# Optimization experiments

Measured on AMD Instinct MI355X. Metric: run time of the kernel, lower is better.

Reference implementation:

```python
import jax, jax.numpy as jnp
import numpy as np

N_UNITS = 512
N_HEADS = 8
CHUNK = N_UNITS // N_HEADS
SCALE = 1.0 / (CHUNK ** 0.5)


def setup_inputs() -> dict:
    key = jax.random.key(0)
    k1, k2, k3, k4, k5, k6 = jax.random.split(key, 6)
    B, Nx, Ny = 8, 1024, 1024
    x = jax.random.normal(k1, (B, N_UNITS, Nx), dtype=jnp.float32)
    y = jax.random.normal(k2, (B, N_UNITS, Ny), dtype=jnp.float32)
    xy_mask = jax.random.randint(k3, (B, Nx, Ny), 0, 2) > 0
    # conv1x1 weight [out, in] (ConvolutionSentence, bias=False)
    W = jax.random.normal(k4, (N_UNITS, N_UNITS), dtype=jnp.float32) * (1.0 / np.sqrt(N_UNITS))
    fc_w = jax.random.normal(k5, (1, N_HEADS), dtype=jnp.float32) * (1.0 / np.sqrt(N_HEADS))
    fc_b = jax.random.normal(k6, (1,), dtype=jnp.float32) * 0.01
    return {"x": x, "y": y, "xy_mask": xy_mask, "W": W, "fc_w": fc_w, "fc_b": fc_b}


def reference(x, y, xy_mask, W, fc_w, fc_b):
    B, U, Nx = x.shape
    Ny = y.shape[2]
    H, C = N_HEADS, CHUNK
    # 1x1 conv over channel dim == linear on channels
    _x = jnp.einsum('oi,bin->bon', W, x)  # [B, U, Nx]
    _y = jnp.einsum('oi,bim->bom', W, y)  # [B, U, Ny]
    # split channels into heads (contiguous chunks, matching torch.split)
    xh = _x.reshape(B, H, C, Nx)
    yh = _y.reshape(B, H, C, Ny)
    # per-head scores: relu, then scale, then mask (order matches torch code)
    s = jnp.einsum('bhcn,bhcm->bhnm', xh, yh)  # [B, H, Nx, Ny]
    s = jnp.maximum(s, 0.0) * SCALE
    s = jnp.where(xy_mask[:, None, :, :], s, 0.0)
    similarity = s.sum(axis=(2, 3))  # [B, H]
    n_el = xy_mask.sum(axis=(1, 2))
    n_el = jnp.where(n_el == 0, 1, n_el).astype(similarity.dtype)
    expectation = similarity / n_el[:, None]
    return expectation @ fc_w.T + fc_b  # [B, 1]
```

## Files before the change

kernel.cpp:

```cpp
#include <hip/hip_runtime.h>
#include <stdint.h>

#define UU 512
#define NHEAD 8
#define NB 8
#define NXX 1024
#define NYY 1024
#define SCALE_F 0.125f

typedef __bf16 bf16x8 __attribute__((ext_vector_type(8)));
typedef float f32x4 __attribute__((ext_vector_type(4)));
typedef unsigned short us4 __attribute__((ext_vector_type(4)));

__device__ __forceinline__ unsigned short f2bf(float f) {
  union { float f; uint32_t u; } v; v.f = f;
  return (unsigned short)((v.u + 0x7FFFu + ((v.u >> 16) & 1u)) >> 16);
}

__global__ void prep_kernel(const float* __restrict__ W, unsigned short* __restrict__ Wp,
                            const unsigned char* __restrict__ m, int* __restrict__ det) {
  int blk = blockIdx.x, t = threadIdx.x;
  if (blk < 128) {
    int s = blk * 256 + t;
    int ub = s >> 10, kb = (s >> 6) & 15, l = s & 63;
    int u = ub * 16 + (l & 15), k = kb * 32 + (l >> 4) * 8;
    const float* src = W + (size_t)u * UU + k;
    float4 a = *(const float4*)src;
    float4 bq = *(const float4*)(src + 4);
    uint4 o;
    o.x = (unsigned)f2bf(a.x) | ((unsigned)f2bf(a.y) << 16);
    o.y = (unsigned)f2bf(a.z) | ((unsigned)f2bf(a.w) << 16);
    o.z = (unsigned)f2bf(bq.x) | ((unsigned)f2bf(bq.y) << 16);
    o.w = (unsigned)f2bf(bq.z) | ((unsigned)f2bf(bq.w) << 16);
    *(uint4*)(Wp + (size_t)s * 8) = o;
  } else {
    int idx = ((blk - 128) * 256 + t) * 16;
    uint4 v = *(const uint4*)(m + idx);
    unsigned int c1 = (v.x & 0xff00u) | (v.y & 0xff00u) | (v.z & 0xff00u) | (v.w & 0xff00u);
    if (c1) atomicOr(&det[0], 1);
  }
}

__global__ __launch_bounds__(256, 2) void conv_fused(
    const float* __restrict__ x, const float* __restrict__ y,
    const unsigned short* __restrict__ Wp, unsigned short* __restrict__ pc) {
  __shared__ unsigned short xs[64 * 512];
  int fl = blockIdx.x;
  int bz = fl & 15, nt = (fl >> 4) & 15, ut = fl >> 8;
  int b = bz & 7;
  const float* src = (bz >> 3) ? y : x;
  int n0 = nt * 64;
  int t = threadIdx.x, w = t >> 6, l = t & 63;
  int lane_m = l & 15, lane_g = l >> 4;

  {
    int cq = (t & 15) * 4;
    int i2b = (t >> 4) * 2;
    const float* gb = src + (size_t)b * UU * NXX + n0 + cq;
#pragma unroll
    for (int it = 0; it < 16; it++) {
      int i2 = i2b + it * 32;
      float4 va = *(const float4*)(gb + (size_t)i2 * NXX);
      float4 vb = *(const float4*)(gb + (size_t)(i2 + 1) * NXX);
      float fa[4] = {va.x, va.y, va.z, va.w};
      float fb[4] = {vb.x, vb.y, vb.z, vb.w};
#pragma unroll
      for (int j = 0; j < 4; j++) {
        int n = cq + j;
        unsigned int pk = (unsigned)f2bf(fa[j]) | ((unsigned)f2bf(fb[j]) << 16);
        int e = n * 512 + (i2 ^ ((n & 7) << 3));
        *(unsigned int*)&xs[e] = pk;
      }
    }
  }
  __syncthreads();

  int u0 = ut * 256 + w * 64;
  int ub0 = u0 >> 4;
  const unsigned short* wb0 = Wp + (size_t)l * 8;
  f32x4 acc[4][4] = {};
  bf16x8 aA[4], aB[4], bA[4], bB[4];

#define LOADW(Adst, Bdst, KB) do {                                            \
    _Pragma("unroll") for (int tu = 0; tu < 4; tu++)                          \
      Adst[tu] = *(const bf16x8*)(wb0 + ((size_t)(ub0 + tu) * 16 + (KB)) * 512); \
    _Pragma("unroll") for (int tn = 0; tn < 4; tn++) {                        \
      int nl_ = tn * 16 + lane_m;                                             \
      int ka_ = (KB) * 32 + lane_g * 8;                                       \
      Bdst[tn] = *(const bf16x8*)&xs[nl_ * 512 + (ka_ ^ ((nl_ & 7) << 3))];   \
    }                                                                         \
  } while (0)
#define DOMFMA(Ab, Bb) do {                                                   \
    _Pragma("unroll") for (int tn = 0; tn < 4; tn++)                          \
    _Pragma("unroll") for (int tu = 0; tu < 4; tu++)                          \
      acc[tn][tu] = __builtin_amdgcn_mfma_f32_16x16x32_bf16(Ab[tu], Bb[tn], acc[tn][tu], 0, 0, 0); \
  } while (0)

  LOADW(aA, bA, 0);
#pragma unroll
  for (int kp = 0; kp < 8; kp++) {
    LOADW(aB, bB, 2 * kp + 1);
    DOMFMA(aA, bA);
    if (kp < 7) LOADW(aA, bA, 2 * kp + 2);
    DOMFMA(aB, bB);
  }
#undef LOADW
#undef DOMFMA

  unsigned short* ob = pc + (size_t)bz * 64 * 8 * 2 * 512;
  int h = u0 >> 6;
  int e0 = 4 * (lane_g & 1);
#pragma unroll
  for (int tn = 0; tn < 4; tn++)
#pragma unroll
    for (int tu = 0; tu < 4; tu++) {
      int q16 = nt * 4 + tn;
      int kb = tu >> 1;
      int g = (2 * tu + (lane_g >> 1)) & 3;
      size_t slot = ((size_t)q16 * 8 + h) * 2 + kb;
      us4 pk;
      pk.x = f2bf(acc[tn][tu][0]); pk.y = f2bf(acc[tn][tu][1]);
      pk.z = f2bf(acc[tn][tu][2]); pk.w = f2bf(acc[tn][tu][3]);
      *(us4*)(ob + slot * 512 + (g * 16 + lane_m) * 8 + e0) = pk;
    }
}

__global__ __launch_bounds__(256, 3) void score_kernel(
    const unsigned short* __restrict__ pc, const void* __restrict__ maskp,
    const int* __restrict__ det, float* __restrict__ part) {
  __shared__ unsigned short mf16[64][72];
  __shared__ float red[4][8];
  int fl = blockIdx.x;
  int b = fl & 7, rr = fl >> 3;
  int nt = rr & 15, mt = rr >> 4;
  int t = threadIdx.x, w = t >> 6, l = t & 63;
  int lane_m = l & 15, lane_g = l >> 4;
  int n0 = nt * 64, m0 = mt * 64;
  int nw0 = (w & 1) * 32, hq = (w >> 1) * 4;

  int is_u8 = det[0] != 0;
  unsigned int cl = 0;
  {
    int row = t >> 2, cq = (t & 3) * 16;
    size_t eb = ((size_t)b * NXX + n0 + row) * NYY + m0 + cq;
    if (is_u8) {
      uint4 v = *(const uint4*)((const unsigned char*)maskp + eb);
#pragma unroll
      for (int j = 0; j < 16; j++) {
        unsigned int word = ((const unsigned int*)&v)[j >> 2];
        int bit = ((word >> ((j & 3) * 8)) & 0xffu) != 0;
        mf16[row][cq + j] = bit ? 0x3F80u : 0u;
        cl += (unsigned)bit;
      }
    } else {
      const unsigned int* mp = (const unsigned int*)maskp + eb;
#pragma unroll
      for (int q = 0; q < 4; q++) {
        uint4 v = *(const uint4*)(mp + q * 4);
        unsigned int wds[4] = {v.x, v.y, v.z, v.w};
#pragma unroll
        for (int j = 0; j < 4; j++) {
          int bit = wds[j] != 0;
          mf16[row][cq + q * 4 + j] = bit ? 0x3F80u : 0u;
          cl += (unsigned)bit;
        }
      }
    }
  }
  for (int s = 1; s < 64; s <<= 1) cl += __shfl_xor(cl, s);
  if (l == 0) red[w][4] = (float)cl;
  __syncthreads();

  float mreg[2][4][4];
#pragma unroll
  for (int tn = 0; tn < 2; tn++)
#pragma unroll
    for (int tm = 0; tm < 4; tm++)
#pragma unroll
      for (int r = 0; r < 4; r++) {
        unsigned int u = (unsigned int)mf16[nw0 + tn * 16 + 4 * lane_g + r][tm * 16 + lane_m] << 16;
        union { unsigned int u; float f; } cvt; cvt.u = u;
        mreg[tn][tm][r] = cvt.f;
      }

  int xq0 = (n0 + nw0) >> 4;
  int yq0 = m0 >> 4;
  const unsigned short* xpl = pc + ((size_t)b * 64) * 8 * 2 * 512 + (size_t)l * 8;
  const unsigned short* ypl = pc + ((size_t)(NB + b) * 64) * 8 * 2 * 512 + (size_t)l * 8;
  float hsv[4] = {0.f, 0.f, 0.f, 0.f};
#pragma unroll
  for (int hh = 0; hh < 4; hh++) {
    int h = hq + hh;
    bf16x8 afr[2][2], bfr[4][2];
#pragma unroll
    for (int tn = 0; tn < 2; tn++)
#pragma unroll
      for (int kb = 0; kb < 2; kb++)
        afr[tn][kb] = *(const bf16x8*)(xpl + ((((size_t)(xq0 + tn)) * 8 + h) * 2 + kb) * 512);
#pragma unroll
    for (int tm = 0; tm < 4; tm++)
#pragma unroll
      for (int kb = 0; kb < 2; kb++)
        bfr[tm][kb] = *(const bf16x8*)(ypl + ((((size_t)(yq0 + tm)) * 8 + h) * 2 + kb) * 512);
#pragma unroll
    for (int tn = 0; tn < 2; tn++)
#pragma unroll
      for (int tm = 0; tm < 4; tm++) {
        f32x4 acc = {};
        acc = __builtin_amdgcn_mfma_f32_16x16x32_bf16(afr[tn][0], bfr[tm][0], acc, 0, 0, 0);
        acc = __builtin_amdgcn_mfma_f32_16x16x32_bf16(afr[tn][1], bfr[tm][1], acc, 0, 0, 0);
#pragma unroll
        for (int r = 0; r < 4; r++) {
          float v = acc[r];
          v = v > 0.f ? v : 0.f;
          hsv[hh] = fmaf(v, mreg[tn][tm][r], hsv[hh]);
        }
      }
  }
#pragma unroll
  for (int hh = 0; hh < 4; hh++) {
    float hs = hsv[hh];
    for (int s = 1; s < 64; s <<= 1) hs += __shfl_xor(hs, s);
    if (l == 0) red[w][hh] = hs;
  }
  __syncthreads();
  float* pb = part + (size_t)fl * 16;
  if (t < 8) {
    int q = t >> 2, hh = t & 3;
    pb[t] = red[q * 2][hh] + red[q * 2 + 1][hh];
  } else if (t == 8) {
    pb[8] = red[0][4] + red[1][4] + red[2][4] + red[3][4];
  }
}

__global__ __launch_bounds__(256) void finalize(
    const float* __restrict__ part, const float* __restrict__ fcw,
    const float* __restrict__ fcb, float* __restrict__ out) {
  __shared__ float red[4][9];
  int b = blockIdx.x;
  int t = threadIdx.x, w = t >> 6, l = t & 63;
  const float* pb = part + (size_t)(t * 8 + b) * 16;
  float v[9];
#pragma unroll
  for (int j = 0; j < 9; j++) v[j] = pb[j];
#pragma unroll
  for (int j = 0; j < 9; j++) {
    float s = v[j];
    for (int ss = 1; ss < 64; ss <<= 1) s += __shfl_xor(s, ss);
    v[j] = s;
  }
  if (l == 0)
#pragma unroll
    for (int j = 0; j < 9; j++) red[w][j] = v[j];
  __syncthreads();
  if (t == 0) {
    float s = 0.f, cn = 0.f;
#pragma unroll
    for (int h = 0; h < NHEAD; h++)
      s += (red[0][h] + red[1][h] + red[2][h] + red[3][h]) * fcw[h];
    cn = red[0][8] + red[1][8] + red[2][8] + red[3][8];
    if (cn < 0.5f) cn = 1.f;
    out[b] = s * (SCALE_F / cn) + fcb[0];
  }
}

extern "C" void kernel_launch(void* const* d_in, const int* in_sizes, int n_in,
                              void* d_out, int out_size, void* d_ws, size_t ws_size,
                              hipStream_t stream) {
  const float* x = (const float*)d_in[0];
  const float* y = (const float*)d_in[1];
  const void* mask = d_in[2];
  const float* W = (const float*)d_in[3];
  const float* fcw = (const float*)d_in[4];
  const float* fcb = (const float*)d_in[5];
  float* out = (float*)d_out;
  char* ws = (char*)d_ws;

  unsigned short* pc = (unsigned short*)ws;
  unsigned short* Wp = (unsigned short*)(ws + (16u << 20));
  float* part = (float*)(ws + (16u << 20) + (1u << 19));
  char* st = ws + (16u << 20) + (1u << 19) + (1u << 17);
  int* det = (int*)st;

  hipMemsetAsync(st, 0, 64, stream);
  prep_kernel<<<144, 256, 0, stream>>>(W, Wp, (const unsigned char*)mask, det);
  conv_fused<<<512, 256, 0, stream>>>(x, y, Wp, pc);
  score_kernel<<<2048, 256, 0, stream>>>(pc, mask, det, part);
  finalize<<<NB, 256, 0, stream>>>(part, fcw, fcb, out);
}
```

Baseline: 142.5 us.

## Precompute bit-packed mask in prep kernel and consume bits in score kernel

The prep kernel now converts the boolean mask (uint8 or int32 layout) into a 64-bit-per-row-segment bitmask, and a separate single-block kernel detects the mask format. The score kernel loads only 64 words of packed mask per tile instead of the full byte mask, uses popcount for the element count, and selects scores by testing bits instead of multiplying by a float mask. This removes the large mask read and the shared-memory expansion from the hot kernel and frees registers, so launch bounds are raised to 4 blocks per CU. The cost is an extra pass over the mask in prep_kernel, which now runs 2176 blocks, plus a serial single-block detection launch.

```diff
diff --git a/kernel.cpp b/kernel.cpp
--- a/kernel.cpp
+++ b/kernel.cpp
@@ -17,8 +17,17 @@
   return (unsigned short)((v.u + 0x7FFFu + ((v.u >> 16) & 1u)) >> 16);
 }
 
+__global__ void detect_mask(const unsigned char* __restrict__ m, int* __restrict__ det) {
+  int t = threadIdx.x;
+  int c1 = 0;
+  for (int q = t; q < 16384; q += 256) c1 |= m[q * 4 + 1];
+  if (c1) atomicOr(&det[0], 1);
+}
+
 __global__ void prep_kernel(const float* __restrict__ W, unsigned short* __restrict__ Wp,
-                            const unsigned char* __restrict__ m, int* __restrict__ det) {
+                            const void* __restrict__ maskp, const int* __restrict__ det,
+                            unsigned long long* __restrict__ mb) {
+  __shared__ unsigned short sm[256];
   int blk = blockIdx.x, t = threadIdx.x;
   if (blk < 128) {
     int s = blk * 256 + t;
@@ -33,11 +42,33 @@
     o.z = (unsigned)f2bf(bq.x) | ((unsigned)f2bf(bq.y) << 16);
     o.w = (unsigned)f2bf(bq.z) | ((unsigned)f2bf(bq.w) << 16);
     *(uint4*)(Wp + (size_t)s * 8) = o;
+    return;
+  }
+  int pb = blk - 128;
+  size_t g = (size_t)pb * 256 + t;
+  unsigned int bm = 0;
+  if (det[0]) {
+    uint4 v = *(const uint4*)((const unsigned char*)maskp + g * 16);
+    unsigned int wd[4] = {v.x, v.y, v.z, v.w};
+#pragma unroll
+    for (int j = 0; j < 16; j++)
+      bm |= (((wd[j >> 2] >> ((j & 3) * 8)) & 0xffu) != 0u) << j;
   } else {
-    int idx = ((blk - 128) * 256 + t) * 16;
-    uint4 v = *(const uint4*)(m + idx);
-    unsigned int c1 = (v.x & 0xff00u) | (v.y & 0xff00u) | (v.z & 0xff00u) | (v.w & 0xff00u);
-    if (c1) atomicOr(&det[0], 1);
+    const unsigned int* mp = (const unsigned int*)maskp + g * 16;
+#pragma unroll
+    for (int q = 0; q < 4; q++) {
+      uint4 v = *(const uint4*)(mp + q * 4);
+      unsigned int wd[4] = {v.x, v.y, v.z, v.w};
+#pragma unroll
+      for (int j = 0; j < 4; j++)
+        bm |= (wd[j] != 0u) << (q * 4 + j);
+    }
+  }
+  sm[t] = (unsigned short)bm;
+  __syncthreads();
+  if (t < 64) {
+    unsigned long long w0 = sm[t * 4], w1 = sm[t * 4 + 1], w2 = sm[t * 4 + 2], w3 = sm[t * 4 + 3];
+    mb[(size_t)pb * 64 + t] = w0 | (w1 << 16) | (w2 << 32) | (w3 << 48);
   }
 }
 
@@ -125,10 +156,10 @@
     }
 }
 
-__global__ __launch_bounds__(256, 3) void score_kernel(
-    const unsigned short* __restrict__ pc, const void* __restrict__ maskp,
-    const int* __restrict__ det, float* __restrict__ part) {
-  __shared__ unsigned short mf16[64][72];
+__global__ __launch_bounds__(256, 4) void score_kernel(
+    const unsigned short* __restrict__ pc, const unsigned long long* __restrict__ mb,
+    float* __restrict__ part) {
+  __shared__ unsigned long long msk[64];
   __shared__ float red[4][8];
   int fl = blockIdx.x;
   int b = fl & 7, rr = fl >> 3;
@@ -138,50 +169,24 @@
   int n0 = nt * 64, m0 = mt * 64;
   int nw0 = (w & 1) * 32, hq = (w >> 1) * 4;
 
-  int is_u8 = det[0] != 0;
-  unsigned int cl = 0;
-  {
-    int row = t >> 2, cq = (t & 3) * 16;
-    size_t eb = ((size_t)b * NXX + n0 + row) * NYY + m0 + cq;
-    if (is_u8) {
-      uint4 v = *(const uint4*)((const unsigned char*)maskp + eb);
-#pragma unroll
-      for (int j = 0; j < 16; j++) {
-        unsigned int word = ((const unsigned int*)&v)[j >> 2];
-        int bit = ((word >> ((j & 3) * 8)) & 0xffu) != 0;
-        mf16[row][cq + j] = bit ? 0x3F80u : 0u;
-        cl += (unsigned)bit;
-      }
-    } else {
-      const unsigned int* mp = (const unsigned int*)maskp + eb;
-#pragma unroll
-      for (int q = 0; q < 4; q++) {
-        uint4 v = *(const uint4*)(mp + q * 4);
-        unsigned int wds[4] = {v.x, v.y, v.z, v.w};
-#pragma unroll
-        for (int j = 0; j < 4; j++) {
-          int bit = wds[j] != 0;
-          mf16[row][cq + q * 4 + j] = bit ? 0x3F80u : 0u;
-          cl += (unsigned)bit;
-        }
-      }
-    }
-  }
-  for (int s = 1; s < 64; s <<= 1) cl += __shfl_xor(cl, s);
-  if (l == 0) red[w][4] = (float)cl;
-  __syncthreads();
-
-  float mreg[2][4][4];
+  if (t < 64) msk[t] = mb[((size_t)b * NXX + n0 + t) * 16 + mt];
+  __syncthreads();
+
+  if (w == 0) {
+    unsigned long long mv = msk[l];
+    unsigned int cl = (unsigned int)__popcll(mv);
+    for (int s = 1; s < 64; s <<= 1) cl += __shfl_xor(cl, s);
+    if (l == 0) red[0][4] = (float)cl;
+  } else if (l == 0) {
+    red[w][4] = 0.f;
+  }
+
+  unsigned long long mw[2][4];
 #pragma unroll
   for (int tn = 0; tn < 2; tn++)
 #pragma unroll
-    for (int tm = 0; tm < 4; tm++)
-#pragma unroll
-      for (int r = 0; r < 4; r++) {
-        unsigned int u = (unsigned int)mf16[nw0 + tn * 16 + 4 * lane_g + r][tm * 16 + lane_m] << 16;
-        union { unsigned int u; float f; } cvt; cvt.u = u;
-        mreg[tn][tm][r] = cvt.f;
-      }
+    for (int r = 0; r < 4; r++)
+      mw[tn][r] = msk[nw0 + tn * 16 + 4 * lane_g + r] >> lane_m;
 
   int xq0 = (n0 + nw0) >> 4;
   int yq0 = m0 >> 4;
@@ -213,7 +218,8 @@
         for (int r = 0; r < 4; r++) {
           float v = acc[r];
           v = v > 0.f ? v : 0.f;
-          hsv[hh] = fmaf(v, mreg[tn][tm][r], hsv[hh]);
+          unsigned int bit = (unsigned int)(mw[tn][r] >> (tm * 16)) & 1u;
+          hsv[hh] += bit ? v : 0.f;
         }
       }
   }
@@ -278,13 +284,14 @@
 
   unsigned short* pc = (unsigned short*)ws;
   unsigned short* Wp = (unsigned short*)(ws + (16u << 20));
-  float* part = (float*)(ws + (16u << 20) + (1u << 19));
-  char* st = ws + (16u << 20) + (1u << 19) + (1u << 17);
-  int* det = (int*)st;
-
-  hipMemsetAsync(st, 0, 64, stream);
-  prep_kernel<<<144, 256, 0, stream>>>(W, Wp, (const unsigned char*)mask, det);
+  float* part = (float*)(ws + (16u << 20) + (512u << 10));
+  unsigned long long* mb = (unsigned long long*)(ws + (16u << 20) + (640u << 10));
+  int* det = (int*)(ws + (16u << 20) + (1664u << 10));
+
+  hipMemsetAsync(det, 0, 64, stream);
+  detect_mask<<<1, 256, 0, stream>>>((const unsigned char*)mask, det);
+  prep_kernel<<<2176, 256, 0, stream>>>(W, Wp, mask, det, mb);
   conv_fused<<<512, 256, 0, stream>>>(x, y, Wp, pc);
-  score_kernel<<<2048, 256, 0, stream>>>(pc, mask, det, part);
+  score_kernel<<<2048, 256, 0, stream>>>(pc, mb, part);
   finalize<<<NB, 256, 0, stream>>>(part, fcw, fcb, out);
 }
```

After: 145.6 us. 1.02x slower.
